# Optimization experiments

Measured on AMD Instinct MI355X. Metric: run time of the kernel, lower is better.

Reference implementation:

```python
import jax, jax.numpy as jnp
import numpy as np
from jax import lax

N, R, W, H = 256, 32, 8, 6       # batch, n_rooms, room width/height
MX, MY = 72, 72                  # map grid
EMB = 6                          # room embedding width
CIN = 10 + EMB                   # conv input channels


def _boundaries(m):
    # m: [R, W, H] binary room masks -> [R, 4, W, H] (left, right, up, down edges)
    left = jnp.concatenate([m[:, :1, :], jnp.clip(m[:, 1:, :] - m[:, :-1, :], 0)], axis=1)
    right = jnp.concatenate([jnp.clip(m[:, :-1, :] - m[:, 1:, :], 0), m[:, -1:, :]], axis=1)
    up = jnp.concatenate([m[:, :, :1], jnp.clip(m[:, :, 1:] - m[:, :, :-1], 0)], axis=2)
    down = jnp.concatenate([jnp.clip(m[:, :, :-1] - m[:, :, 1:], 0), m[:, :, -1:]], axis=2)
    return jnp.stack([left, right, up, down], axis=1)


def setup_inputs() -> dict:
    key = jax.random.key(0)
    ks = jax.random.split(key, 12)
    room_map = (jax.random.uniform(ks[0], (R, W, H)) < 0.7).astype(jnp.float32)
    room_map = room_map.at[:, 0, 0].set(1.0)  # guarantee nonempty rooms
    doors = (jax.random.uniform(ks[1], (R, 4, W, H)) < 0.15).astype(jnp.float32) * room_map[:, None]
    room_tensor = jnp.concatenate([room_map[:, None], doors, _boundaries(room_map)], axis=1)  # [R,9,W,H]
    px = jax.random.randint(ks[2], (N, R), 0, MX - W)
    py = jax.random.randint(ks[3], (N, R), 0, MY - H)
    room_positions = jnp.stack([px, py], axis=-1).astype(jnp.int32)  # [N,R,2]

    def rn(k, shape, fan_in):
        return jax.random.normal(k, shape, jnp.float32) / np.float32(np.sqrt(fan_in))

    inp = dict(room_positions=room_positions, room_tensor=room_tensor)
    inp['room_embedding'] = jax.random.normal(ks[4], (R, EMB), jnp.float32)
    inp['w_conv1'] = rn(ks[5], (64, CIN, 5, 5), CIN * 25); inp['b_conv1'] = jnp.zeros((64,), jnp.float32)
    inp['w_conv2'] = rn(ks[6], (64, 64, 3, 3), 64 * 9);    inp['b_conv2'] = jnp.zeros((64,), jnp.float32)
    inp['w_conv3'] = rn(ks[7], (64, 64, 3, 3), 64 * 9);    inp['b_conv3'] = jnp.zeros((64,), jnp.float32)
    inp['w_room1'] = rn(ks[8], (128, 64), 64);   inp['b_room1'] = jnp.zeros((128,), jnp.float32)
    inp['w_room2'] = rn(ks[9], (128, 128), 128); inp['b_room2'] = jnp.zeros((128,), jnp.float32)
    inp['w_fc1'] = rn(ks[10], (256, 128), 128);  inp['b_fc1'] = jnp.zeros((256,), jnp.float32)
    inp['w_fc2'] = rn(ks[11], (256, 256), 256);  inp['b_fc2'] = jnp.zeros((256,), jnp.float32)
    return inp


def _conv2d_relu(x, w, b):
    pad = w.shape[-1] // 2
    y = lax.conv_general_dilated(x, w, (1, 1), [(pad, pad), (pad, pad)],
                                 dimension_numbers=('NCHW', 'OIHW', 'NCHW'))
    return jax.nn.relu(y + b[None, :, None, None])


def _forward(room_positions, room_tensor, room_embedding,
             w_conv1, b_conv1, w_conv2, b_conv2, w_conv3, b_conv3,
             w_room1, b_room1, w_room2, b_room2, w_fc1, b_fc1, w_fc2, b_fc2):
    room_map = room_tensor[:, 0]                      # [R,W,H]
    px = room_positions[..., 0]                       # [N,R]
    py = room_positions[..., 1]
    # ---- encode_map: scatter-add all rooms into grid ----
    bidx = jnp.arange(N)[:, None, None, None, None]
    cidx = jnp.arange(9)[None, None, :, None, None]
    ix = px[:, :, None, None, None] + jnp.arange(W)[None, None, None, :, None]   # [N,R,1,W,1]
    iy = py[:, :, None, None, None] + jnp.arange(H)[None, None, None, None, :]   # [N,R,1,1,H]
    map9 = jnp.zeros((N, 9, MX, MY), jnp.float32).at[bidx, cidx, ix, iy].add(room_tensor[None])
    eidx = jnp.arange(EMB)[None, None, :, None, None]
    evals = room_embedding[:, :, None, None] * room_map[:, None, :, :]           # [R,EMB,W,H]
    embg = jnp.zeros((N, EMB, MX, MY), jnp.float32).at[bidx, eidx, ix, iy].add(evals[None])
    X = jnp.concatenate([map9, jnp.ones((N, 1, MX, MY), jnp.float32), embg], axis=1)  # [N,16,MX,MY]
    # ---- map convs ----
    X = _conv2d_relu(X, w_conv1, b_conv1)
    X = _conv2d_relu(X, w_conv2, b_conv2)
    X = _conv2d_relu(X, w_conv3, b_conv3)
    # ---- decode_map: gather room tiles, masked mean per room ----
    Xt = jnp.transpose(X, (0, 2, 3, 1))                                          # [N,MX,MY,C]
    g = Xt[jnp.arange(N)[:, None, None, None],
           px[:, :, None, None] + jnp.arange(W)[None, None, :, None],
           py[:, :, None, None] + jnp.arange(H)[None, None, None, :]]            # [N,R,W,H,C]
    g = g * room_map[None, :, :, :, None]
    room_feat = g.sum(axis=(2, 3)) / room_map.sum(axis=(1, 2))[None, :, None]    # [N,R,C]
    X = jnp.transpose(room_feat, (0, 2, 1))                                      # [N,C,R]
    # ---- 1x1 conv1d room layers ----
    X = jax.nn.relu(jnp.einsum('ncr,oc->nor', X, w_room1) + b_room1[None, :, None])
    X = jax.nn.relu(jnp.einsum('ncr,oc->nor', X, w_room2) + b_room2[None, :, None])
    # ---- fc head: sum over rooms, MLP ----
    X = X.sum(axis=2)                                                            # [N,128]
    X = jax.nn.relu(X @ w_fc1.T + b_fc1)
    return X @ w_fc2.T + b_fc2                                                   # [N,256]


def reference(room_positions, room_tensor, room_embedding,
              w_conv1, b_conv1, w_conv2, b_conv2, w_conv3, b_conv3,
              w_room1, b_room1, w_room2, b_room2, w_fc1, b_fc1, w_fc2, b_fc2):
    return _forward(room_positions, room_tensor, room_embedding,
                    w_conv1, b_conv1, w_conv2, b_conv2, w_conv3, b_conv3,
                    w_room1, b_room1, w_room2, b_room2, w_fc1, b_fc1, w_fc2, b_fc2)
```

## Files before the change

### kernel.cpp

```cpp
#include <hip/hip_runtime.h>
#include <hip/hip_bf16.h>
#include <cstddef>

#define NB 256
#define RR 32
#define WW 8
#define HH 6
#define MXY 72
#define EMB 6
#define CIN1 16

typedef __bf16 bf16x8 __attribute__((ext_vector_type(8)));
typedef float floatx4 __attribute__((ext_vector_type(4)));

static const size_t B_W1F  = 0;
static const size_t B_W2F  = 57344;
static const size_t B_W3F  = 131072;
static const size_t B_RAUX = 204800;
static const size_t B_RINV = 205056;
static const size_t B_HEAD = 205312;
static const size_t F_WR1T = 0;
static const size_t F_WR2T = 8192;
static const size_t F_F1T  = 24576;
static const size_t F_F2T  = 57344;
static const size_t B_FEAT = 696832;
static const size_t B_CHUNK = 2793984;
static const size_t PERN_BYTES = 165888;

__device__ inline short f2b(float f) {
    unsigned u = __builtin_bit_cast(unsigned, f);
    unsigned r = (u + 0x7fffu + ((u >> 16) & 1u)) >> 16;
    return (short)r;
}

__global__ void prep_weights(const float* __restrict__ w1, const float* __restrict__ w2,
                             const float* __restrict__ w3, const float* __restrict__ wr1,
                             const float* __restrict__ wr2, const float* __restrict__ wf1,
                             const float* __restrict__ wf2, char* __restrict__ ws)
{
    short* W1F = (short*)(ws + B_W1F);
    short* W2F = (short*)(ws + B_W2F);
    short* W3F = (short*)(ws + B_W3F);
    float* HEAD = (float*)(ws + B_HEAD);

    int idx = blockIdx.x * 256 + threadIdx.x;
    if (idx < 28672) {
        int j = idx & 7, lane = (idx >> 3) & 63, nt = (idx >> 9) & 3, kk = idx >> 11;
        int k = kk * 32 + (lane >> 4) * 8 + j;
        int oc = nt * 16 + (lane & 15);
        int tap = k >> 4, ci = k & 15;
        float v = (tap < 25) ? w1[(oc * 16 + ci) * 25 + tap] : 0.f;
        W1F[idx] = f2b(v);
        return;
    }
    idx -= 28672;
    if (idx < 36864) {
        int j = idx & 7, lane = (idx >> 3) & 63, nt = (idx >> 9) & 3, kk = idx >> 11;
        int k = kk * 32 + (lane >> 4) * 8 + j;
        int oc = nt * 16 + (lane & 15);
        int tap = k >> 6, cp = k & 63;
        int ci = (cp >> 2) + (cp & 3) * 16;
        W2F[idx] = f2b(w2[(oc * 64 + ci) * 9 + tap]);
        return;
    }
    idx -= 36864;
    if (idx < 36864) {
        int j = idx & 7, lane = (idx >> 3) & 63, nt = (idx >> 9) & 3, kk = idx >> 11;
        int k = kk * 32 + (lane >> 4) * 8 + j;
        int oc = nt * 16 + (lane & 15);
        int tap = k >> 6, cp = k & 63;
        int ci = (cp >> 2) + (cp & 3) * 16;
        W3F[idx] = f2b(w3[(oc * 64 + ci) * 9 + tap]);
        return;
    }
    idx -= 36864;
    if (idx < 8192)  { int o = idx & 127, c = idx >> 7; HEAD[F_WR1T + idx] = wr1[o * 64 + c]; return; }
    idx -= 8192;
    if (idx < 16384) { int o = idx & 127, c = idx >> 7; HEAD[F_WR2T + idx] = wr2[o * 128 + c]; return; }
    idx -= 16384;
    if (idx < 32768) { int o = idx & 255, c = idx >> 8; HEAD[F_F1T + idx] = wf1[o * 128 + c]; return; }
    idx -= 32768;
    if (idx < 65536) { int o = idx & 255, c = idx >> 8; HEAD[F_F2T + idx] = wf2[o * 256 + c]; return; }
}

__global__ void prep_rooms(const float* __restrict__ rt, char* __restrict__ ws)
{
    int r = threadIdx.x;
    if (r >= RR) return;
    unsigned long long m = 0ull;
    int cnt = 0;
    for (int j = 0; j < WW * HH; ++j)
        if (rt[r * 9 * 48 + j] != 0.f) { m |= (1ull << j); ++cnt; }
    ((unsigned long long*)(ws + B_RAUX))[r] = m;
    ((float*)(ws + B_RINV))[r] = 1.f / (float)cnt;
}

__global__ __launch_bounds__(256) void build_x(const int* __restrict__ pos,
                                               const float* __restrict__ rt,
                                               const float* __restrict__ emb,
                                               short* __restrict__ X, int n0)
{
    const int nl = blockIdx.y;
    const int n = n0 + nl;
    const int p = blockIdx.x * 256 + threadIdx.x;

    __shared__ int s_px[RR], s_py[RR];
    __shared__ float s_emb[RR * EMB];
    if (threadIdx.x < RR) {
        s_px[threadIdx.x] = pos[(n * RR + threadIdx.x) * 2 + 0];
        s_py[threadIdx.x] = pos[(n * RR + threadIdx.x) * 2 + 1];
    }
    for (int i = threadIdx.x; i < RR * EMB; i += 256) s_emb[i] = emb[i];
    __syncthreads();
    if (p >= MXY * MXY) return;

    const int gx = p / MXY, gy = p - (p / MXY) * MXY;

    float acc[16];
#pragma unroll
    for (int c = 0; c < 16; ++c) acc[c] = 0.f;
    acc[9] = 1.f;

    for (int r = 0; r < RR; ++r) {
        int w = gx - s_px[r], h = gy - s_py[r];
        if ((unsigned)w < (unsigned)WW && (unsigned)h < (unsigned)HH) {
            int j = w * HH + h;
            const float* rr = rt + r * 9 * 48;
#pragma unroll
            for (int c = 0; c < 9; ++c) acc[c] += rr[c * 48 + j];
            float m = rr[j];
#pragma unroll
            for (int e = 0; e < EMB; ++e) acc[10 + e] += s_emb[r * EMB + e] * m;
        }
    }

    short o[16];
#pragma unroll
    for (int c = 0; c < 16; ++c) o[c] = f2b(acc[c]);
    short* dst = X + ((size_t)nl * (MXY * MXY) + p) * CIN1;
    *reinterpret_cast<uint4*>(dst) = *reinterpret_cast<uint4*>(o);
    *reinterpret_cast<uint4*>(dst + 8) = *reinterpret_cast<uint4*>(o + 8);
}

__global__ __launch_bounds__(256, 3) void fused_conv(const short* __restrict__ X,
    const short* __restrict__ wAll, const float* __restrict__ bc1,
    const float* __restrict__ bc2, const float* __restrict__ bc3,
    const int* __restrict__ pos, const unsigned long long* __restrict__ rmask,
    float* __restrict__ feat, int n0)
{
    __shared__ __align__(16) short s_Y1[120 * 72];
    __shared__ __align__(16) short s_u[80 * 72];
    __shared__ __align__(16) short s_B[2][4096];
    __shared__ float s_feat[64];

    const int tid = threadIdx.x;
    const int lane = tid & 63;
    const int wv = tid >> 6;
    const int ml = lane & 15;
    const int q = lane >> 4;
    const int room = blockIdx.x;
    const int nl = blockIdx.y;
    const int n = n0 + nl;

    const int px = pos[(n * RR + room) * 2 + 0];
    const int py = pos[(n * RR + room) * 2 + 1];

    const char* wB = (const char*)wAll;
    auto dma = [&](int ph) {
        const char* src = wB + (size_t)ph * 8192 + wv * 2048 + lane * 16;
        short* d0 = &s_B[ph & 1][wv * 1024];
        __builtin_amdgcn_global_load_lds(
            (const __attribute__((address_space(1))) unsigned int*)src,
            (__attribute__((address_space(3))) unsigned int*)d0, 16, 0, 0);
        __builtin_amdgcn_global_load_lds(
            (const __attribute__((address_space(1))) unsigned int*)(src + 1024),
            (__attribute__((address_space(3))) unsigned int*)(d0 + 512), 16, 0, 0);
    };

    dma(0);

    const short* Xn = X + (size_t)nl * (MXY * MXY) * CIN1;
    for (int i = tid; i < 448; i += 256) {
        int half = i & 1, pix = i >> 1;
        int row = pix / 14, col = pix - row * 14;
        int gx = px - 4 + row, gy = py - 4 + col;
        uint4 v = make_uint4(0u, 0u, 0u, 0u);
        if ((unsigned)gx < (unsigned)MXY && (unsigned)gy < (unsigned)MXY)
            v = *reinterpret_cast<const uint4*>(Xn + ((size_t)gx * MXY + gy) * CIN1 + half * 8);
        *reinterpret_cast<uint4*>(&s_u[pix * 24 + half * 8]) = v;
    }
    __syncthreads();

    {
        int prow[2], pcol[2];
#pragma unroll
        for (int i = 0; i < 2; ++i) {
            int p = wv * 32 + i * 16 + ml;
            if (p > 119) p = 119;
            prow[i] = p / 10; pcol[i] = p - prow[i] * 10;
        }
        floatx4 acc1[2][4] = {};

#pragma unroll
        for (int t = 0; t < 7; ++t) {
            dma(t + 1);
            const short* sb = s_B[t & 1];
#pragma unroll
            for (int kb = 0; kb < 2; ++kb) {
                const int kk = t * 2 + kb;
                bf16x8 Bf[4];
#pragma unroll
                for (int j2 = 0; j2 < 4; ++j2)
                    Bf[j2] = *reinterpret_cast<const bf16x8*>(&sb[kb * 2048 + (j2 * 64 + lane) * 8]);
                int tap = kk * 2 + (q >> 1);
                if (tap > 24) tap = 24;
                const int chb = (q & 1) * 8;
                const int dx = tap / 5, dy = tap - (tap / 5) * 5;
                __builtin_amdgcn_s_setprio(1);
#pragma unroll
                for (int i = 0; i < 2; ++i) {
                    bf16x8 A = *reinterpret_cast<const bf16x8*>(
                        &s_u[((prow[i] + dx) * 14 + (pcol[i] + dy)) * 24 + chb]);
#pragma unroll
                    for (int j2 = 0; j2 < 4; ++j2)
                        acc1[i][j2] = __builtin_amdgcn_mfma_f32_16x16x32_bf16(
                            A, Bf[j2], acc1[i][j2], 0, 0, 0);
                }
                __builtin_amdgcn_s_setprio(0);
            }
            if (t == 6) {
                float b4[4];
#pragma unroll
                for (int j2 = 0; j2 < 4; ++j2) b4[j2] = bc1[j2 * 16 + ml];
#pragma unroll
                for (int i = 0; i < 2; ++i)
#pragma unroll
                    for (int r = 0; r < 4; ++r) {
                        int p = wv * 32 + i * 16 + q * 4 + r;
                        if (p < 120) {
                            unsigned lo = (unsigned)(unsigned short)f2b(fmaxf(acc1[i][0][r] + b4[0], 0.f))
                                        | ((unsigned)(unsigned short)f2b(fmaxf(acc1[i][1][r] + b4[1], 0.f)) << 16);
                            unsigned hi = (unsigned)(unsigned short)f2b(fmaxf(acc1[i][2][r] + b4[2], 0.f))
                                        | ((unsigned)(unsigned short)f2b(fmaxf(acc1[i][3][r] + b4[3], 0.f)) << 16);
                            *reinterpret_cast<uint2*>(&s_Y1[p * 72 + ml * 4]) = make_uint2(lo, hi);
                        }
                    }
            }
            __syncthreads();
        }
    }

    {
        int prowA, pcolA, prowB, pcolB;
        {
            int p0 = wv * 16 + ml; prowA = p0 >> 3; pcolA = p0 & 7;
            int p1 = 64 + ml;      prowB = p1 >> 3; pcolB = p1 & 7;
        }
        floatx4 acc2[4] = {};
        floatx4 acc2t = {};

#pragma unroll
        for (int t = 0; t < 9; ++t) {
            dma(8 + t);
            const short* sb = s_B[(7 + t) & 1];
#pragma unroll
            for (int kb = 0; kb < 2; ++kb) {
                const int kk = t * 2 + kb;
                bf16x8 Bf[4];
#pragma unroll
                for (int j2 = 0; j2 < 4; ++j2)
                    Bf[j2] = *reinterpret_cast<const bf16x8*>(&sb[kb * 2048 + (j2 * 64 + lane) * 8]);
                bf16x8 B4 = *reinterpret_cast<const bf16x8*>(&sb[kb * 2048 + (wv * 64 + lane) * 8]);
                const int tap = kk >> 1;
                const int chb = (kk & 1) * 32 + q * 8;
                const int dx = tap / 3, dy = tap - (tap / 3) * 3;
                bf16x8 A0 = *reinterpret_cast<const bf16x8*>(
                    &s_Y1[((prowA + dx) * 10 + (pcolA + dy)) * 72 + chb]);
                bf16x8 A4 = *reinterpret_cast<const bf16x8*>(
                    &s_Y1[((prowB + dx) * 10 + (pcolB + dy)) * 72 + chb]);
                __builtin_amdgcn_s_setprio(1);
#pragma unroll
                for (int j2 = 0; j2 < 4; ++j2)
                    acc2[j2] = __builtin_amdgcn_mfma_f32_16x16x32_bf16(A0, Bf[j2], acc2[j2], 0, 0, 0);
                acc2t = __builtin_amdgcn_mfma_f32_16x16x32_bf16(A4, B4, acc2t, 0, 0, 0);
                __builtin_amdgcn_s_setprio(0);
            }
            if (t == 8) {
                float b4[4];
#pragma unroll
                for (int j2 = 0; j2 < 4; ++j2) b4[j2] = bc2[j2 * 16 + ml];
#pragma unroll
                for (int r = 0; r < 4; ++r) {
                    int p = wv * 16 + q * 4 + r;
                    unsigned lo = (unsigned)(unsigned short)f2b(fmaxf(acc2[0][r] + b4[0], 0.f))
                                | ((unsigned)(unsigned short)f2b(fmaxf(acc2[1][r] + b4[1], 0.f)) << 16);
                    unsigned hi = (unsigned)(unsigned short)f2b(fmaxf(acc2[2][r] + b4[2], 0.f))
                                | ((unsigned)(unsigned short)f2b(fmaxf(acc2[3][r] + b4[3], 0.f)) << 16);
                    *reinterpret_cast<uint2*>(&s_u[p * 72 + ml * 4]) = make_uint2(lo, hi);
                }
                float bt = bc2[wv * 16 + ml];
#pragma unroll
                for (int r = 0; r < 4; ++r) {
                    int p = 64 + q * 4 + r;
                    s_u[p * 72 + ml * 4 + wv] = f2b(fmaxf(acc2t[r] + bt, 0.f));
                }
                if (tid < 64) s_feat[tid] = 0.f;
            }
            __syncthreads();
        }
    }

    {
        int prow3, pcol3;
        {
            int p0 = wv * 16 + ml;
            prow3 = p0 / 6; pcol3 = p0 - prow3 * 6;
        }
        floatx4 acc3[4] = {};

#pragma unroll
        for (int t = 0; t < 9; ++t) {
            if (t < 8) dma(17 + t);
            const short* sb = s_B[(16 + t) & 1];
            if (wv < 3) {
#pragma unroll
                for (int kb = 0; kb < 2; ++kb) {
                    const int kk = t * 2 + kb;
                    bf16x8 Bf[4];
#pragma unroll
                    for (int j2 = 0; j2 < 4; ++j2)
                        Bf[j2] = *reinterpret_cast<const bf16x8*>(&sb[kb * 2048 + (j2 * 64 + lane) * 8]);
                    const int tap = kk >> 1;
                    const int chb = (kk & 1) * 32 + q * 8;
                    const int dx = tap / 3, dy = tap - (tap / 3) * 3;
                    bf16x8 A = *reinterpret_cast<const bf16x8*>(
                        &s_u[((prow3 + dx) * 8 + (pcol3 + dy)) * 72 + chb]);
                    __builtin_amdgcn_s_setprio(1);
#pragma unroll
                    for (int j2 = 0; j2 < 4; ++j2)
                        acc3[j2] = __builtin_amdgcn_mfma_f32_16x16x32_bf16(A, Bf[j2], acc3[j2], 0, 0, 0);
                    __builtin_amdgcn_s_setprio(0);
                }
            }
            if (t == 8 && wv < 3) {
                float b4[4];
#pragma unroll
                for (int j2 = 0; j2 < 4; ++j2) b4[j2] = bc3[j2 * 16 + ml];
                float part[4] = {0.f, 0.f, 0.f, 0.f};
                const unsigned long long mk = rmask[room];
#pragma unroll
                for (int r = 0; r < 4; ++r) {
                    int p = wv * 16 + q * 4 + r;
                    if ((mk >> p) & 1ull) {
#pragma unroll
                        for (int j2 = 0; j2 < 4; ++j2)
                            part[j2] += fmaxf(acc3[j2][r] + b4[j2], 0.f);
                    }
                }
#pragma unroll
                for (int j2 = 0; j2 < 4; ++j2) {
                    part[j2] += __shfl_xor(part[j2], 16);
                    part[j2] += __shfl_xor(part[j2], 32);
                }
                if (q == 0) {
#pragma unroll
                    for (int j2 = 0; j2 < 4; ++j2)
                        atomicAdd(&s_feat[j2 * 16 + ml], part[j2]);
                }
            }
            __syncthreads();
        }
    }

    if (tid < 64)
        feat[((size_t)n * RR + room) * 64 + tid] = s_feat[tid];
}

__global__ __launch_bounds__(256) void mlp_head(const float* __restrict__ feat,
                                                const float* __restrict__ HEAD,
                                                const float* __restrict__ rinv,
                                                const float* __restrict__ b1,
                                                const float* __restrict__ b2,
                                                const float* __restrict__ bf1,
                                                const float* __restrict__ bf2,
                                                float* __restrict__ outp)
{
    __shared__ __align__(16) float s_feat[RR * 64];
    __shared__ __align__(16) float s_h1[RR * 128];
    __shared__ __align__(16) float s_s[2 * 128];
    __shared__ __align__(16) float s_sf[128];
    __shared__ __align__(16) float s_t1[256];

    const int n = blockIdx.x;
    const int tid = threadIdx.x;
    const float* W1t = HEAD + F_WR1T;
    const float* W2t = HEAD + F_WR2T;
    const float* F1t = HEAD + F_F1T;
    const float* F2t = HEAD + F_F2T;

    for (int i = tid; i < RR * 64; i += 256)
        s_feat[i] = feat[(size_t)n * RR * 64 + i] * rinv[i >> 6];
    __syncthreads();

    const int o = tid & 127;
    const int rh = tid >> 7;

    float acc[16];
#pragma unroll
    for (int r = 0; r < 16; ++r) acc[r] = b1[o];
    for (int c4 = 0; c4 < 16; ++c4) {
        float w0 = W1t[(c4 * 4 + 0) * 128 + o];
        float w1 = W1t[(c4 * 4 + 1) * 128 + o];
        float w2 = W1t[(c4 * 4 + 2) * 128 + o];
        float w3 = W1t[(c4 * 4 + 3) * 128 + o];
#pragma unroll
        for (int r = 0; r < 16; ++r) {
            float4 f = *reinterpret_cast<const float4*>(&s_feat[(rh * 16 + r) * 64 + c4 * 4]);
            acc[r] += f.x * w0 + f.y * w1 + f.z * w2 + f.w * w3;
        }
    }
#pragma unroll
    for (int r = 0; r < 16; ++r) s_h1[(rh * 16 + r) * 128 + o] = fmaxf(acc[r], 0.f);
    __syncthreads();

#pragma unroll
    for (int r = 0; r < 16; ++r) acc[r] = b2[o];
    for (int c4 = 0; c4 < 32; ++c4) {
        float w0 = W2t[(c4 * 4 + 0) * 128 + o];
        float w1 = W2t[(c4 * 4 + 1) * 128 + o];
        float w2 = W2t[(c4 * 4 + 2) * 128 + o];
        float w3 = W2t[(c4 * 4 + 3) * 128 + o];
#pragma unroll
        for (int r = 0; r < 16; ++r) {
            float4 f = *reinterpret_cast<const float4*>(&s_h1[(rh * 16 + r) * 128 + c4 * 4]);
            acc[r] += f.x * w0 + f.y * w1 + f.z * w2 + f.w * w3;
        }
    }
    float ps = 0.f;
#pragma unroll
    for (int r = 0; r < 16; ++r) ps += fmaxf(acc[r], 0.f);
    s_s[rh * 128 + o] = ps;
    __syncthreads();
    if (tid < 128) s_sf[tid] = s_s[tid] + s_s[128 + tid];
    __syncthreads();

    {
        float a = bf1[tid];
        for (int c4 = 0; c4 < 32; ++c4) {
            float4 f = *reinterpret_cast<const float4*>(&s_sf[c4 * 4]);
            a += f.x * F1t[(c4 * 4 + 0) * 256 + tid];
            a += f.y * F1t[(c4 * 4 + 1) * 256 + tid];
            a += f.z * F1t[(c4 * 4 + 2) * 256 + tid];
            a += f.w * F1t[(c4 * 4 + 3) * 256 + tid];
        }
        s_t1[tid] = fmaxf(a, 0.f);
    }
    __syncthreads();

    {
        float a = bf2[tid];
        for (int c4 = 0; c4 < 64; ++c4) {
            float4 f = *reinterpret_cast<const float4*>(&s_t1[c4 * 4]);
            a += f.x * F2t[(c4 * 4 + 0) * 256 + tid];
            a += f.y * F2t[(c4 * 4 + 1) * 256 + tid];
            a += f.z * F2t[(c4 * 4 + 2) * 256 + tid];
            a += f.w * F2t[(c4 * 4 + 3) * 256 + tid];
        }
        outp[(size_t)n * 256 + tid] = a;
    }
}

extern "C" void kernel_launch(void* const* d_in, const int* in_sizes, int n_in,
                              void* d_out, int out_size, void* d_ws, size_t ws_size,
                              hipStream_t stream)
{
    const int* pos = (const int*)d_in[0];
    const float* rt = (const float*)d_in[1];
    const float* emb = (const float*)d_in[2];
    const float* w1 = (const float*)d_in[3];
    const float* bc1 = (const float*)d_in[4];
    const float* w2 = (const float*)d_in[5];
    const float* bc2 = (const float*)d_in[6];
    const float* w3 = (const float*)d_in[7];
    const float* bc3 = (const float*)d_in[8];
    const float* wr1 = (const float*)d_in[9];
    const float* br1 = (const float*)d_in[10];
    const float* wr2 = (const float*)d_in[11];
    const float* br2 = (const float*)d_in[12];
    const float* wf1 = (const float*)d_in[13];
    const float* bf1 = (const float*)d_in[14];
    const float* wf2 = (const float*)d_in[15];
    const float* bf2 = (const float*)d_in[16];
    float* out = (float*)d_out;
    char* ws = (char*)d_ws;

    prep_weights<<<880, 256, 0, stream>>>(w1, w2, w3, wr1, wr2, wf1, wf2, ws);
    prep_rooms<<<1, 64, 0, stream>>>(rt, ws);

    int nc = 16;
    const int cands[4] = {256, 128, 64, 32};
    for (int k = 0; k < 4; ++k) {
        size_t need = B_CHUNK + (size_t)cands[k] * PERN_BYTES;
        if (need <= ws_size) { nc = cands[k]; break; }
    }

    const short* WALL = (const short*)(ws + B_W1F);
    const unsigned long long* RMASK = (const unsigned long long*)(ws + B_RAUX);
    const float* RINV = (const float*)(ws + B_RINV);
    float* HEAD = (float*)(ws + B_HEAD);
    float* FEAT = (float*)(ws + B_FEAT);
    short* Xc = (short*)(ws + B_CHUNK);

    for (int n0 = 0; n0 < NB; n0 += nc) {
        build_x<<<dim3(21, nc), 256, 0, stream>>>(pos, rt, emb, Xc, n0);
        fused_conv<<<dim3(RR, nc), 256, 0, stream>>>(Xc, WALL, bc1, bc2, bc3,
                                                     pos, RMASK, FEAT, n0);
    }

    mlp_head<<<NB, 256, 0, stream>>>(FEAT, HEAD, RINV, br1, br2, bf1, bf2, out);
}
```

Before: 313.3 us.

## Process two batch samples per fused_conv block to amortize weight loads and balance waves

```diff
diff --git a/kernel.cpp b/kernel.cpp
--- a/kernel.cpp
+++ b/kernel.cpp
@@ -142,16 +142,16 @@
     *reinterpret_cast<uint4*>(dst + 8) = *reinterpret_cast<uint4*>(o + 8);
 }
 
-__global__ __launch_bounds__(256, 3) void fused_conv(const short* __restrict__ X,
+__global__ __launch_bounds__(256, 2) void fused_conv(const short* __restrict__ X,
     const short* __restrict__ wAll, const float* __restrict__ bc1,
     const float* __restrict__ bc2, const float* __restrict__ bc3,
     const int* __restrict__ pos, const unsigned long long* __restrict__ rmask,
     float* __restrict__ feat, int n0)
 {
-    __shared__ __align__(16) short s_Y1[120 * 72];
-    __shared__ __align__(16) short s_u[80 * 72];
+    __shared__ __align__(16) short s_Y1[2 * 8640];
+    __shared__ __align__(16) short s_u[2 * 5760];
     __shared__ __align__(16) short s_B[2][4096];
-    __shared__ float s_feat[64];
+    __shared__ float s_feat[2][64];
 
     const int tid = threadIdx.x;
     const int lane = tid & 63;
@@ -159,11 +159,14 @@
     const int ml = lane & 15;
     const int q = lane >> 4;
     const int room = blockIdx.x;
-    const int nl = blockIdx.y;
-    const int n = n0 + nl;
-
-    const int px = pos[(n * RR + room) * 2 + 0];
-    const int py = pos[(n * RR + room) * 2 + 1];
+    const int pair = blockIdx.y;
+    const int lA = 2 * pair;
+    const int nA = n0 + lA;
+
+    const int pxA = pos[(nA * RR + room) * 2 + 0];
+    const int pyA = pos[(nA * RR + room) * 2 + 1];
+    const int pxB = pos[((nA + 1) * RR + room) * 2 + 0];
+    const int pyB = pos[((nA + 1) * RR + room) * 2 + 1];
 
     const char* wB = (const char*)wAll;
     auto dma = [&](int ph) {
@@ -179,35 +182,41 @@
 
     dma(0);
 
-    const short* Xn = X + (size_t)nl * (MXY * MXY) * CIN1;
-    for (int i = tid; i < 448; i += 256) {
-        int half = i & 1, pix = i >> 1;
+    for (int i = tid; i < 896; i += 256) {
+        int smp = (i >= 448);
+        int ii = i - (smp ? 448 : 0);
+        int half = ii & 1, pix = ii >> 1;
         int row = pix / 14, col = pix - row * 14;
-        int gx = px - 4 + row, gy = py - 4 + col;
+        int gx = (smp ? pxB : pxA) - 4 + row;
+        int gy = (smp ? pyB : pyA) - 4 + col;
+        const short* Xn = X + (size_t)(lA + smp) * (MXY * MXY) * CIN1;
         uint4 v = make_uint4(0u, 0u, 0u, 0u);
         if ((unsigned)gx < (unsigned)MXY && (unsigned)gy < (unsigned)MXY)
             v = *reinterpret_cast<const uint4*>(Xn + ((size_t)gx * MXY + gy) * CIN1 + half * 8);
-        *reinterpret_cast<uint4*>(&s_u[pix * 24 + half * 8]) = v;
+        *reinterpret_cast<uint4*>(&s_u[smp * 5760 + pix * 24 + half * 8]) = v;
     }
     __syncthreads();
 
     {
-        int prow[2], pcol[2];
-#pragma unroll
-        for (int i = 0; i < 2; ++i) {
-            int p = wv * 32 + i * 16 + ml;
+        int pr1[4], pc1[4], sm1[4];
+#pragma unroll
+        for (int k = 0; k < 4; ++k) {
+            int s = wv + 4 * k;
+            int t = s & 7;
+            int p = t * 16 + ml;
             if (p > 119) p = 119;
-            prow[i] = p / 10; pcol[i] = p - prow[i] * 10;
-        }
-        floatx4 acc1[2][4] = {};
-
-#pragma unroll
-        for (int t = 0; t < 7; ++t) {
-            dma(t + 1);
-            const short* sb = s_B[t & 1];
+            pr1[k] = p / 10; pc1[k] = p - (p / 10) * 10;
+            sm1[k] = (s >> 3) * 5760;
+        }
+        floatx4 acc1[4][4] = {};
+
+#pragma unroll
+        for (int t7 = 0; t7 < 7; ++t7) {
+            dma(t7 + 1);
+            const short* sb = s_B[t7 & 1];
 #pragma unroll
             for (int kb = 0; kb < 2; ++kb) {
-                const int kk = t * 2 + kb;
+                const int kk = t7 * 2 + kb;
                 bf16x8 Bf[4];
 #pragma unroll
                 for (int j2 = 0; j2 < 4; ++j2)
@@ -218,143 +227,168 @@
                 const int dx = tap / 5, dy = tap - (tap / 5) * 5;
                 __builtin_amdgcn_s_setprio(1);
 #pragma unroll
-                for (int i = 0; i < 2; ++i) {
+                for (int k = 0; k < 4; ++k) {
                     bf16x8 A = *reinterpret_cast<const bf16x8*>(
-                        &s_u[((prow[i] + dx) * 14 + (pcol[i] + dy)) * 24 + chb]);
+                        &s_u[sm1[k] + ((pr1[k] + dx) * 14 + (pc1[k] + dy)) * 24 + chb]);
 #pragma unroll
                     for (int j2 = 0; j2 < 4; ++j2)
-                        acc1[i][j2] = __builtin_amdgcn_mfma_f32_16x16x32_bf16(
-                            A, Bf[j2], acc1[i][j2], 0, 0, 0);
+                        acc1[k][j2] = __builtin_amdgcn_mfma_f32_16x16x32_bf16(
+                            A, Bf[j2], acc1[k][j2], 0, 0, 0);
                 }
                 __builtin_amdgcn_s_setprio(0);
             }
-            if (t == 6) {
+            if (t7 == 6) {
                 float b4[4];
 #pragma unroll
                 for (int j2 = 0; j2 < 4; ++j2) b4[j2] = bc1[j2 * 16 + ml];
 #pragma unroll
-                for (int i = 0; i < 2; ++i)
+                for (int k = 0; k < 4; ++k) {
+                    int s = wv + 4 * k;
+                    int t = s & 7;
+                    int sy = (s >> 3) * 8640;
 #pragma unroll
                     for (int r = 0; r < 4; ++r) {
-                        int p = wv * 32 + i * 16 + q * 4 + r;
+                        int p = t * 16 + q * 4 + r;
                         if (p < 120) {
-                            unsigned lo = (unsigned)(unsigned short)f2b(fmaxf(acc1[i][0][r] + b4[0], 0.f))
-                                        | ((unsigned)(unsigned short)f2b(fmaxf(acc1[i][1][r] + b4[1], 0.f)) << 16);
-                            unsigned hi = (unsigned)(unsigned short)f2b(fmaxf(acc1[i][2][r] + b4[2], 0.f))
-                                        | ((unsigned)(unsigned short)f2b(fmaxf(acc1[i][3][r] + b4[3], 0.f)) << 16);
-                            *reinterpret_cast<uint2*>(&s_Y1[p * 72 + ml * 4]) = make_uint2(lo, hi);
+                            unsigned lo = (unsigned)(unsigned short)f2b(fmaxf(acc1[k][0][r] + b4[0], 0.f))
+                                        | ((unsigned)(unsigned short)f2b(fmaxf(acc1[k][1][r] + b4[1], 0.f)) << 16);
+                            unsigned hi = (unsigned)(unsigned short)f2b(fmaxf(acc1[k][2][r] + b4[2], 0.f))
+                                        | ((unsigned)(unsigned short)f2b(fmaxf(acc1[k][3][r] + b4[3], 0.f)) << 16);
+                            *reinterpret_cast<uint2*>(&s_Y1[sy + p * 72 + ml * 4]) = make_uint2(lo, hi);
                         }
                     }
+                }
             }
             __syncthreads();
         }
     }
 
     {
-        int prowA, pcolA, prowB, pcolB;
-        {
-            int p0 = wv * 16 + ml; prowA = p0 >> 3; pcolA = p0 & 7;
-            int p1 = 64 + ml;      prowB = p1 >> 3; pcolB = p1 & 7;
-        }
-        floatx4 acc2[4] = {};
-        floatx4 acc2t = {};
-
-#pragma unroll
-        for (int t = 0; t < 9; ++t) {
-            dma(8 + t);
-            const short* sb = s_B[(7 + t) & 1];
+        int prA[3], pcA[3], smY[3], smU[3], t2[3];
+#pragma unroll
+        for (int k = 0; k < 3; ++k) {
+            int s = wv + 4 * k;
+            int sm = s / 6;
+            int t = s - sm * 6;
+            int te = (t == 5) ? 4 : t;
+            int p = te * 16 + ml;
+            prA[k] = p >> 3; pcA[k] = p & 7;
+            smY[k] = sm * 8640;
+            smU[k] = sm * 5760;
+            t2[k] = t;
+        }
+        floatx4 acc2[3][4] = {};
+
+#pragma unroll
+        for (int t9 = 0; t9 < 9; ++t9) {
+            dma(8 + t9);
+            const short* sb = s_B[(7 + t9) & 1];
 #pragma unroll
             for (int kb = 0; kb < 2; ++kb) {
-                const int kk = t * 2 + kb;
+                const int kk = t9 * 2 + kb;
                 bf16x8 Bf[4];
 #pragma unroll
                 for (int j2 = 0; j2 < 4; ++j2)
                     Bf[j2] = *reinterpret_cast<const bf16x8*>(&sb[kb * 2048 + (j2 * 64 + lane) * 8]);
-                bf16x8 B4 = *reinterpret_cast<const bf16x8*>(&sb[kb * 2048 + (wv * 64 + lane) * 8]);
                 const int tap = kk >> 1;
                 const int chb = (kk & 1) * 32 + q * 8;
                 const int dx = tap / 3, dy = tap - (tap / 3) * 3;
-                bf16x8 A0 = *reinterpret_cast<const bf16x8*>(
-                    &s_Y1[((prowA + dx) * 10 + (pcolA + dy)) * 72 + chb]);
-                bf16x8 A4 = *reinterpret_cast<const bf16x8*>(
-                    &s_Y1[((prowB + dx) * 10 + (pcolB + dy)) * 72 + chb]);
                 __builtin_amdgcn_s_setprio(1);
 #pragma unroll
-                for (int j2 = 0; j2 < 4; ++j2)
-                    acc2[j2] = __builtin_amdgcn_mfma_f32_16x16x32_bf16(A0, Bf[j2], acc2[j2], 0, 0, 0);
-                acc2t = __builtin_amdgcn_mfma_f32_16x16x32_bf16(A4, B4, acc2t, 0, 0, 0);
+                for (int k = 0; k < 3; ++k) {
+                    bf16x8 A = *reinterpret_cast<const bf16x8*>(
+                        &s_Y1[smY[k] + ((prA[k] + dx) * 10 + (pcA[k] + dy)) * 72 + chb]);
+#pragma unroll
+                    for (int j2 = 0; j2 < 4; ++j2)
+                        acc2[k][j2] = __builtin_amdgcn_mfma_f32_16x16x32_bf16(
+                            A, Bf[j2], acc2[k][j2], 0, 0, 0);
+                }
                 __builtin_amdgcn_s_setprio(0);
             }
-            if (t == 8) {
+            if (t9 == 8) {
                 float b4[4];
 #pragma unroll
                 for (int j2 = 0; j2 < 4; ++j2) b4[j2] = bc2[j2 * 16 + ml];
 #pragma unroll
-                for (int r = 0; r < 4; ++r) {
-                    int p = wv * 16 + q * 4 + r;
-                    unsigned lo = (unsigned)(unsigned short)f2b(fmaxf(acc2[0][r] + b4[0], 0.f))
-                                | ((unsigned)(unsigned short)f2b(fmaxf(acc2[1][r] + b4[1], 0.f)) << 16);
-                    unsigned hi = (unsigned)(unsigned short)f2b(fmaxf(acc2[2][r] + b4[2], 0.f))
-                                | ((unsigned)(unsigned short)f2b(fmaxf(acc2[3][r] + b4[3], 0.f)) << 16);
-                    *reinterpret_cast<uint2*>(&s_u[p * 72 + ml * 4]) = make_uint2(lo, hi);
-                }
-                float bt = bc2[wv * 16 + ml];
-#pragma unroll
-                for (int r = 0; r < 4; ++r) {
-                    int p = 64 + q * 4 + r;
-                    s_u[p * 72 + ml * 4 + wv] = f2b(fmaxf(acc2t[r] + bt, 0.f));
-                }
-                if (tid < 64) s_feat[tid] = 0.f;
+                for (int k = 0; k < 3; ++k) {
+                    if (t2[k] != 5) {
+#pragma unroll
+                        for (int r = 0; r < 4; ++r) {
+                            int p = t2[k] * 16 + q * 4 + r;
+                            unsigned lo = (unsigned)(unsigned short)f2b(fmaxf(acc2[k][0][r] + b4[0], 0.f))
+                                        | ((unsigned)(unsigned short)f2b(fmaxf(acc2[k][1][r] + b4[1], 0.f)) << 16);
+                            unsigned hi = (unsigned)(unsigned short)f2b(fmaxf(acc2[k][2][r] + b4[2], 0.f))
+                                        | ((unsigned)(unsigned short)f2b(fmaxf(acc2[k][3][r] + b4[3], 0.f)) << 16);
+                            *reinterpret_cast<uint2*>(&s_u[smU[k] + p * 72 + ml * 4]) = make_uint2(lo, hi);
+                        }
+                    }
+                }
+                if (tid < 128) s_feat[tid >> 6][tid & 63] = 0.f;
             }
             __syncthreads();
         }
     }
 
     {
-        int prow3, pcol3;
-        {
-            int p0 = wv * 16 + ml;
-            prow3 = p0 / 6; pcol3 = p0 - prow3 * 6;
-        }
-        floatx4 acc3[4] = {};
-
-#pragma unroll
-        for (int t = 0; t < 9; ++t) {
-            if (t < 8) dma(17 + t);
-            const short* sb = s_B[(16 + t) & 1];
-            if (wv < 3) {
-#pragma unroll
-                for (int kb = 0; kb < 2; ++kb) {
-                    const int kk = t * 2 + kb;
-                    bf16x8 Bf[4];
+        int pr3[2], pc3[2], smU3[2], smF3[2], t3[2];
+#pragma unroll
+        for (int k = 0; k < 2; ++k) {
+            int s = wv + 4 * k;
+            int sm = s >> 2;
+            int t = s & 3;
+            int te = (t == 3) ? 2 : t;
+            int p = te * 16 + ml;
+            pr3[k] = p / 6; pc3[k] = p - (p / 6) * 6;
+            smU3[k] = sm * 5760;
+            smF3[k] = sm;
+            t3[k] = t;
+        }
+        floatx4 acc3[2][4] = {};
+
+#pragma unroll
+        for (int t9 = 0; t9 < 9; ++t9) {
+            if (t9 < 8) dma(17 + t9);
+            const short* sb = s_B[(16 + t9) & 1];
+#pragma unroll
+            for (int kb = 0; kb < 2; ++kb) {
+                const int kk = t9 * 2 + kb;
+                bf16x8 Bf[4];
+#pragma unroll
+                for (int j2 = 0; j2 < 4; ++j2)
+                    Bf[j2] = *reinterpret_cast<const bf16x8*>(&sb[kb * 2048 + (j2 * 64 + lane) * 8]);
+                const int tap = kk >> 1;
+                const int chb = (kk & 1) * 32 + q * 8;
+                const int dx = tap / 3, dy = tap - (tap / 3) * 3;
+                __builtin_amdgcn_s_setprio(1);
+#pragma unroll
+                for (int k = 0; k < 2; ++k) {
+                    bf16x8 A = *reinterpret_cast<const bf16x8*>(
+                        &s_u[smU3[k] + ((pr3[k] + dx) * 8 + (pc3[k] + dy)) * 72 + chb]);
 #pragma unroll
                     for (int j2 = 0; j2 < 4; ++j2)
-                        Bf[j2] = *reinterpret_cast<const bf16x8*>(&sb[kb * 2048 + (j2 * 64 + lane) * 8]);
-                    const int tap = kk >> 1;
-                    const int chb = (kk & 1) * 32 + q * 8;
-                    const int dx = tap / 3, dy = tap - (tap / 3) * 3;
-                    bf16x8 A = *reinterpret_cast<const bf16x8*>(
-                        &s_u[((prow3 + dx) * 8 + (pcol3 + dy)) * 72 + chb]);
-                    __builtin_amdgcn_s_setprio(1);
-#pragma unroll
-                    for (int j2 = 0; j2 < 4; ++j2)
-                        acc3[j2] = __builtin_amdgcn_mfma_f32_16x16x32_bf16(A, Bf[j2], acc3[j2], 0, 0, 0);
-                    __builtin_amdgcn_s_setprio(0);
-                }
+                        acc3[k][j2] = __builtin_amdgcn_mfma_f32_16x16x32_bf16(
+                            A, Bf[j2], acc3[k][j2], 0, 0, 0);
+                }
+                __builtin_amdgcn_s_setprio(0);
             }
-            if (t == 8 && wv < 3) {
-                float b4[4];
-#pragma unroll
-                for (int j2 = 0; j2 < 4; ++j2) b4[j2] = bc3[j2 * 16 + ml];
+            if (t9 < 8) __syncthreads();
+        }
+
+        float b4[4];
+#pragma unroll
+        for (int j2 = 0; j2 < 4; ++j2) b4[j2] = bc3[j2 * 16 + ml];
+        const unsigned long long mk = rmask[room];
+#pragma unroll
+        for (int k = 0; k < 2; ++k) {
+            if (t3[k] != 3) {
                 float part[4] = {0.f, 0.f, 0.f, 0.f};
-                const unsigned long long mk = rmask[room];
 #pragma unroll
                 for (int r = 0; r < 4; ++r) {
-                    int p = wv * 16 + q * 4 + r;
+                    int p = t3[k] * 16 + q * 4 + r;
                     if ((mk >> p) & 1ull) {
 #pragma unroll
                         for (int j2 = 0; j2 < 4; ++j2)
-                            part[j2] += fmaxf(acc3[j2][r] + b4[j2], 0.f);
+                            part[j2] += fmaxf(acc3[k][j2][r] + b4[j2], 0.f);
                     }
                 }
 #pragma unroll
@@ -365,15 +399,16 @@
                 if (q == 0) {
 #pragma unroll
                     for (int j2 = 0; j2 < 4; ++j2)
-                        atomicAdd(&s_feat[j2 * 16 + ml], part[j2]);
+                        atomicAdd(&s_feat[smF3[k]][j2 * 16 + ml], part[j2]);
                 }
             }
-            __syncthreads();
-        }
-    }
-
-    if (tid < 64)
-        feat[((size_t)n * RR + room) * 64 + tid] = s_feat[tid];
+        }
+    }
+    __syncthreads();
+
+    if (tid < 128)
+        feat[((size_t)(nA + (tid >> 6)) * RR + room) * 64 + (tid & 63)] =
+            s_feat[tid >> 6][tid & 63];
 }
 
 __global__ __launch_bounds__(256) void mlp_head(const float* __restrict__ feat,
@@ -513,8 +548,8 @@
 
     for (int n0 = 0; n0 < NB; n0 += nc) {
         build_x<<<dim3(21, nc), 256, 0, stream>>>(pos, rt, emb, Xc, n0);
-        fused_conv<<<dim3(RR, nc), 256, 0, stream>>>(Xc, WALL, bc1, bc2, bc3,
-                                                     pos, RMASK, FEAT, n0);
+        fused_conv<<<dim3(RR, nc / 2), 256, 0, stream>>>(Xc, WALL, bc1, bc2, bc3,
+                                                         pos, RMASK, FEAT, n0);
     }
 
     mlp_head<<<NB, 256, 0, stream>>>(FEAT, HEAD, RINV, br1, br2, bf1, bf2, out);
```

Result: faster. 303.4 us (-3.2%).

## Load conv weights directly into registers instead of LDS double-buffer

Applied to the files above, without the earlier changes.

```diff
diff --git a/kernel.cpp b/kernel.cpp
--- a/kernel.cpp
+++ b/kernel.cpp
@@ -142,7 +142,7 @@
     *reinterpret_cast<uint4*>(dst + 8) = *reinterpret_cast<uint4*>(o + 8);
 }
 
-__global__ __launch_bounds__(256, 3) void fused_conv(const short* __restrict__ X,
+__global__ __launch_bounds__(256, 5) void fused_conv(const short* __restrict__ X,
     const short* __restrict__ wAll, const float* __restrict__ bc1,
     const float* __restrict__ bc2, const float* __restrict__ bc3,
     const int* __restrict__ pos, const unsigned long long* __restrict__ rmask,
@@ -150,7 +150,6 @@
 {
     __shared__ __align__(16) short s_Y1[120 * 72];
     __shared__ __align__(16) short s_u[80 * 72];
-    __shared__ __align__(16) short s_B[2][4096];
     __shared__ float s_feat[64];
 
     const int tid = threadIdx.x;
@@ -165,19 +164,23 @@
     const int px = pos[(n * RR + room) * 2 + 0];
     const int py = pos[(n * RR + room) * 2 + 1];
 
-    const char* wB = (const char*)wAll;
-    auto dma = [&](int ph) {
-        const char* src = wB + (size_t)ph * 8192 + wv * 2048 + lane * 16;
-        short* d0 = &s_B[ph & 1][wv * 1024];
-        __builtin_amdgcn_global_load_lds(
-            (const __attribute__((address_space(1))) unsigned int*)src,
-            (__attribute__((address_space(3))) unsigned int*)d0, 16, 0, 0);
-        __builtin_amdgcn_global_load_lds(
-            (const __attribute__((address_space(1))) unsigned int*)(src + 1024),
-            (__attribute__((address_space(3))) unsigned int*)(d0 + 512), 16, 0, 0);
+    const short* W1F = wAll;
+    const short* W2F = wAll + B_W2F / 2;
+    const short* W3F = wAll + B_W3F / 2;
+
+    bf16x8 Bb[2][4];
+    bf16x8 B4b[2];
+    auto load_k = [&](const short* wF, int kk, bf16x8* dst) {
+        const short* src = wF + (size_t)kk * 2048;
+#pragma unroll
+        for (int j2 = 0; j2 < 4; ++j2)
+            dst[j2] = *reinterpret_cast<const bf16x8*>(src + (j2 * 64 + lane) * 8);
     };
-
-    dma(0);
+    auto load_b4 = [&](const short* wF, int kk, bf16x8* dst) {
+        *dst = *reinterpret_cast<const bf16x8*>(wF + (size_t)kk * 2048 + (wv * 64 + lane) * 8);
+    };
+
+    load_k(W1F, 0, Bb[0]);
 
     const short* Xn = X + (size_t)nl * (MXY * MXY) * CIN1;
     for (int i = tid; i < 448; i += 256) {
@@ -202,53 +205,43 @@
         floatx4 acc1[2][4] = {};
 
 #pragma unroll
-        for (int t = 0; t < 7; ++t) {
-            dma(t + 1);
-            const short* sb = s_B[t & 1];
-#pragma unroll
-            for (int kb = 0; kb < 2; ++kb) {
-                const int kk = t * 2 + kb;
-                bf16x8 Bf[4];
+        for (int kk = 0; kk < 13; ++kk) {
+            if (kk < 12) { load_k(W1F, kk + 1, Bb[(kk + 1) & 1]); }
+            else         { load_k(W2F, 0, Bb[1]); load_b4(W2F, 0, &B4b[1]); }
+            int tap = kk * 2 + (q >> 1);
+            if (tap > 24) tap = 24;
+            int chb = (q & 1) * 8;
+            int dx = tap / 5, dy = tap - dx * 5;
+            __builtin_amdgcn_s_setprio(1);
+#pragma unroll
+            for (int i = 0; i < 2; ++i) {
+                bf16x8 A = *reinterpret_cast<const bf16x8*>(
+                    &s_u[((prow[i] + dx) * 14 + (pcol[i] + dy)) * 24 + chb]);
 #pragma unroll
                 for (int j2 = 0; j2 < 4; ++j2)
-                    Bf[j2] = *reinterpret_cast<const bf16x8*>(&sb[kb * 2048 + (j2 * 64 + lane) * 8]);
-                int tap = kk * 2 + (q >> 1);
-                if (tap > 24) tap = 24;
-                const int chb = (q & 1) * 8;
-                const int dx = tap / 5, dy = tap - (tap / 5) * 5;
-                __builtin_amdgcn_s_setprio(1);
-#pragma unroll
-                for (int i = 0; i < 2; ++i) {
-                    bf16x8 A = *reinterpret_cast<const bf16x8*>(
-                        &s_u[((prow[i] + dx) * 14 + (pcol[i] + dy)) * 24 + chb]);
-#pragma unroll
-                    for (int j2 = 0; j2 < 4; ++j2)
-                        acc1[i][j2] = __builtin_amdgcn_mfma_f32_16x16x32_bf16(
-                            A, Bf[j2], acc1[i][j2], 0, 0, 0);
+                    acc1[i][j2] = __builtin_amdgcn_mfma_f32_16x16x32_bf16(
+                        A, Bb[kk & 1][j2], acc1[i][j2], 0, 0, 0);
+            }
+            __builtin_amdgcn_s_setprio(0);
+        }
+        float b4[4];
+#pragma unroll
+        for (int j2 = 0; j2 < 4; ++j2) b4[j2] = bc1[j2 * 16 + ml];
+#pragma unroll
+        for (int i = 0; i < 2; ++i)
+#pragma unroll
+            for (int r = 0; r < 4; ++r) {
+                int p = wv * 32 + i * 16 + q * 4 + r;
+                if (p < 120) {
+                    unsigned lo = (unsigned)(unsigned short)f2b(fmaxf(acc1[i][0][r] + b4[0], 0.f))
+                                | ((unsigned)(unsigned short)f2b(fmaxf(acc1[i][1][r] + b4[1], 0.f)) << 16);
+                    unsigned hi = (unsigned)(unsigned short)f2b(fmaxf(acc1[i][2][r] + b4[2], 0.f))
+                                | ((unsigned)(unsigned short)f2b(fmaxf(acc1[i][3][r] + b4[3], 0.f)) << 16);
+                    *reinterpret_cast<uint2*>(&s_Y1[p * 72 + ml * 4]) = make_uint2(lo, hi);
                 }
-                __builtin_amdgcn_s_setprio(0);
             }
-            if (t == 6) {
-                float b4[4];
-#pragma unroll
-                for (int j2 = 0; j2 < 4; ++j2) b4[j2] = bc1[j2 * 16 + ml];
-#pragma unroll
-                for (int i = 0; i < 2; ++i)
-#pragma unroll
-                    for (int r = 0; r < 4; ++r) {
-                        int p = wv * 32 + i * 16 + q * 4 + r;
-                        if (p < 120) {
-                            unsigned lo = (unsigned)(unsigned short)f2b(fmaxf(acc1[i][0][r] + b4[0], 0.f))
-                                        | ((unsigned)(unsigned short)f2b(fmaxf(acc1[i][1][r] + b4[1], 0.f)) << 16);
-                            unsigned hi = (unsigned)(unsigned short)f2b(fmaxf(acc1[i][2][r] + b4[2], 0.f))
-                                        | ((unsigned)(unsigned short)f2b(fmaxf(acc1[i][3][r] + b4[3], 0.f)) << 16);
-                            *reinterpret_cast<uint2*>(&s_Y1[p * 72 + ml * 4]) = make_uint2(lo, hi);
-                        }
-                    }
-            }
-            __syncthreads();
-        }
-    }
+    }
+    __syncthreads();
 
     {
         int prowA, pcolA, prowB, pcolB;
@@ -257,121 +250,95 @@
             int p1 = 64 + ml;      prowB = p1 >> 3; pcolB = p1 & 7;
         }
         floatx4 acc2[4] = {};
-        floatx4 acc2t = {};
-
-#pragma unroll
-        for (int t = 0; t < 9; ++t) {
-            dma(8 + t);
-            const short* sb = s_B[(7 + t) & 1];
-#pragma unroll
-            for (int kb = 0; kb < 2; ++kb) {
-                const int kk = t * 2 + kb;
-                bf16x8 Bf[4];
+        floatx4 acc2s = {};
+
+#pragma unroll
+        for (int kk = 0; kk < 18; ++kk) {
+            if (kk < 17) { load_k(W2F, kk + 1, Bb[kk & 1]); load_b4(W2F, kk + 1, &B4b[kk & 1]); }
+            else         { load_k(W3F, 0, Bb[1]); }
+            const int tap = kk >> 1;
+            const int chb = (kk & 1) * 32 + q * 8;
+            const int dx = tap / 3, dy = tap - (tap / 3) * 3;
+            bf16x8 A0 = *reinterpret_cast<const bf16x8*>(
+                &s_Y1[((prowA + dx) * 10 + (pcolA + dy)) * 72 + chb]);
+            bf16x8 A4 = *reinterpret_cast<const bf16x8*>(
+                &s_Y1[((prowB + dx) * 10 + (pcolB + dy)) * 72 + chb]);
+            __builtin_amdgcn_s_setprio(1);
+#pragma unroll
+            for (int j2 = 0; j2 < 4; ++j2)
+                acc2[j2] = __builtin_amdgcn_mfma_f32_16x16x32_bf16(A0, Bb[(kk + 1) & 1][j2], acc2[j2], 0, 0, 0);
+            acc2s = __builtin_amdgcn_mfma_f32_16x16x32_bf16(A4, B4b[(kk + 1) & 1], acc2s, 0, 0, 0);
+            __builtin_amdgcn_s_setprio(0);
+        }
+        float b4[4];
+#pragma unroll
+        for (int j2 = 0; j2 < 4; ++j2) b4[j2] = bc2[j2 * 16 + ml];
+#pragma unroll
+        for (int r = 0; r < 4; ++r) {
+            int p = wv * 16 + q * 4 + r;
+            unsigned lo = (unsigned)(unsigned short)f2b(fmaxf(acc2[0][r] + b4[0], 0.f))
+                        | ((unsigned)(unsigned short)f2b(fmaxf(acc2[1][r] + b4[1], 0.f)) << 16);
+            unsigned hi = (unsigned)(unsigned short)f2b(fmaxf(acc2[2][r] + b4[2], 0.f))
+                        | ((unsigned)(unsigned short)f2b(fmaxf(acc2[3][r] + b4[3], 0.f)) << 16);
+            *reinterpret_cast<uint2*>(&s_u[p * 72 + ml * 4]) = make_uint2(lo, hi);
+        }
+        {
+            float bt = bc2[wv * 16 + ml];
+#pragma unroll
+            for (int r = 0; r < 4; ++r) {
+                int p = 64 + q * 4 + r;
+                s_u[p * 72 + ml * 4 + wv] = f2b(fmaxf(acc2s[r] + bt, 0.f));
+            }
+        }
+        if (tid < 64) s_feat[tid] = 0.f;
+    }
+    __syncthreads();
+
+    if (wv < 3) {
+        int p0 = wv * 16 + ml;
+        int row3 = p0 / 6, col3 = p0 - (p0 / 6) * 6;
+        floatx4 acc3[4] = {};
+
+#pragma unroll
+        for (int kk = 0; kk < 18; ++kk) {
+            if (kk < 17) load_k(W3F, kk + 1, Bb[kk & 1]);
+            const int tap = kk >> 1;
+            const int chb = (kk & 1) * 32 + q * 8;
+            const int dx = tap / 3, dy = tap - (tap / 3) * 3;
+            bf16x8 A = *reinterpret_cast<const bf16x8*>(
+                &s_u[((row3 + dx) * 8 + (col3 + dy)) * 72 + chb]);
+            __builtin_amdgcn_s_setprio(1);
+#pragma unroll
+            for (int j2 = 0; j2 < 4; ++j2)
+                acc3[j2] = __builtin_amdgcn_mfma_f32_16x16x32_bf16(A, Bb[(kk + 1) & 1][j2], acc3[j2], 0, 0, 0);
+            __builtin_amdgcn_s_setprio(0);
+        }
+        float b4[4];
+#pragma unroll
+        for (int j2 = 0; j2 < 4; ++j2) b4[j2] = bc3[j2 * 16 + ml];
+        float part[4] = {0.f, 0.f, 0.f, 0.f};
+        const unsigned long long mk = rmask[room];
+#pragma unroll
+        for (int r = 0; r < 4; ++r) {
+            int p = wv * 16 + q * 4 + r;
+            if ((mk >> p) & 1ull) {
 #pragma unroll
                 for (int j2 = 0; j2 < 4; ++j2)
-                    Bf[j2] = *reinterpret_cast<const bf16x8*>(&sb[kb * 2048 + (j2 * 64 + lane) * 8]);
-                bf16x8 B4 = *reinterpret_cast<const bf16x8*>(&sb[kb * 2048 + (wv * 64 + lane) * 8]);
-                const int tap = kk >> 1;
-                const int chb = (kk & 1) * 32 + q * 8;
-                const int dx = tap / 3, dy = tap - (tap / 3) * 3;
-                bf16x8 A0 = *reinterpret_cast<const bf16x8*>(
-                    &s_Y1[((prowA + dx) * 10 + (pcolA + dy)) * 72 + chb]);
-                bf16x8 A4 = *reinterpret_cast<const bf16x8*>(
-                    &s_Y1[((prowB + dx) * 10 + (pcolB + dy)) * 72 + chb]);
-                __builtin_amdgcn_s_setprio(1);
-#pragma unroll
-                for (int j2 = 0; j2 < 4; ++j2)
-                    acc2[j2] = __builtin_amdgcn_mfma_f32_16x16x32_bf16(A0, Bf[j2], acc2[j2], 0, 0, 0);
-                acc2t = __builtin_amdgcn_mfma_f32_16x16x32_bf16(A4, B4, acc2t, 0, 0, 0);
-                __builtin_amdgcn_s_setprio(0);
+                    part[j2] += fmaxf(acc3[j2][r] + b4[j2], 0.f);
             }
-            if (t == 8) {
-                float b4[4];
-#pragma unroll
-                for (int j2 = 0; j2 < 4; ++j2) b4[j2] = bc2[j2 * 16 + ml];
-#pragma unroll
-                for (int r = 0; r < 4; ++r) {
-                    int p = wv * 16 + q * 4 + r;
-                    unsigned lo = (unsigned)(unsigned short)f2b(fmaxf(acc2[0][r] + b4[0], 0.f))
-                                | ((unsigned)(unsigned short)f2b(fmaxf(acc2[1][r] + b4[1], 0.f)) << 16);
-                    unsigned hi = (unsigned)(unsigned short)f2b(fmaxf(acc2[2][r] + b4[2], 0.f))
-                                | ((unsigned)(unsigned short)f2b(fmaxf(acc2[3][r] + b4[3], 0.f)) << 16);
-                    *reinterpret_cast<uint2*>(&s_u[p * 72 + ml * 4]) = make_uint2(lo, hi);
-                }
-                float bt = bc2[wv * 16 + ml];
-#pragma unroll
-                for (int r = 0; r < 4; ++r) {
-                    int p = 64 + q * 4 + r;
-                    s_u[p * 72 + ml * 4 + wv] = f2b(fmaxf(acc2t[r] + bt, 0.f));
-                }
-                if (tid < 64) s_feat[tid] = 0.f;
-            }
-            __syncthreads();
-        }
-    }
-
-    {
-        int prow3, pcol3;
-        {
-            int p0 = wv * 16 + ml;
-            prow3 = p0 / 6; pcol3 = p0 - prow3 * 6;
-        }
-        floatx4 acc3[4] = {};
-
-#pragma unroll
-        for (int t = 0; t < 9; ++t) {
-            if (t < 8) dma(17 + t);
-            const short* sb = s_B[(16 + t) & 1];
-            if (wv < 3) {
-#pragma unroll
-                for (int kb = 0; kb < 2; ++kb) {
-                    const int kk = t * 2 + kb;
-                    bf16x8 Bf[4];
-#pragma unroll
-                    for (int j2 = 0; j2 < 4; ++j2)
-                        Bf[j2] = *reinterpret_cast<const bf16x8*>(&sb[kb * 2048 + (j2 * 64 + lane) * 8]);
-                    const int tap = kk >> 1;
-                    const int chb = (kk & 1) * 32 + q * 8;
-                    const int dx = tap / 3, dy = tap - (tap / 3) * 3;
-                    bf16x8 A = *reinterpret_cast<const bf16x8*>(
-                        &s_u[((prow3 + dx) * 8 + (pcol3 + dy)) * 72 + chb]);
-                    __builtin_amdgcn_s_setprio(1);
-#pragma unroll
-                    for (int j2 = 0; j2 < 4; ++j2)
-                        acc3[j2] = __builtin_amdgcn_mfma_f32_16x16x32_bf16(A, Bf[j2], acc3[j2], 0, 0, 0);
-                    __builtin_amdgcn_s_setprio(0);
-                }
-            }
-            if (t == 8 && wv < 3) {
-                float b4[4];
-#pragma unroll
-                for (int j2 = 0; j2 < 4; ++j2) b4[j2] = bc3[j2 * 16 + ml];
-                float part[4] = {0.f, 0.f, 0.f, 0.f};
-                const unsigned long long mk = rmask[room];
-#pragma unroll
-                for (int r = 0; r < 4; ++r) {
-                    int p = wv * 16 + q * 4 + r;
-                    if ((mk >> p) & 1ull) {
-#pragma unroll
-                        for (int j2 = 0; j2 < 4; ++j2)
-                            part[j2] += fmaxf(acc3[j2][r] + b4[j2], 0.f);
-                    }
-                }
-#pragma unroll
-                for (int j2 = 0; j2 < 4; ++j2) {
-                    part[j2] += __shfl_xor(part[j2], 16);
-                    part[j2] += __shfl_xor(part[j2], 32);
-                }
-                if (q == 0) {
-#pragma unroll
-                    for (int j2 = 0; j2 < 4; ++j2)
-                        atomicAdd(&s_feat[j2 * 16 + ml], part[j2]);
-                }
-            }
-            __syncthreads();
-        }
-    }
-
+        }
+#pragma unroll
+        for (int j2 = 0; j2 < 4; ++j2) {
+            part[j2] += __shfl_xor(part[j2], 16);
+            part[j2] += __shfl_xor(part[j2], 32);
+        }
+        if (q == 0) {
+#pragma unroll
+            for (int j2 = 0; j2 < 4; ++j2)
+                atomicAdd(&s_feat[j2 * 16 + ml], part[j2]);
+        }
+    }
+    __syncthreads();
     if (tid < 64)
         feat[((size_t)n * RR + room) * 64 + tid] = s_feat[tid];
 }
```

Result: slower. 349.5 us (+11.5%).
